# Optimization experiments

Measured on AMD Instinct MI355X. Metric: run time of the kernel, lower is better.

## Reference

```python
import jax, jax.numpy as jnp
import numpy as np

T, B = 32, 64
D_IN = 512      # input_size == embedding dim
H = 512         # hidden_size
V = 32000       # n_vocab
F_FEAT = 768    # feature_size
NH = 8          # num_heads
HD = H // NH    # head_dim


def setup_inputs() -> dict:
    key = jax.random.key(0)
    ks = jax.random.split(key, 16)
    s = 0.02
    inp = {
        'y': jax.random.randint(ks[0], (T, B), 0, V),
        'ctx': jax.random.normal(ks[1], (1, B, F_FEAT), jnp.float32),
        'emb_W': jax.random.normal(ks[2], (V, D_IN), jnp.float32) * s,
        # GRUCell dec0: gates ordered (r, z, n) as in torch
        'W_ih': jax.random.normal(ks[3], (3 * H, D_IN), jnp.float32) * s,
        'b_ih': jnp.zeros((3 * H,), jnp.float32),
        'W_hh': jax.random.normal(ks[4], (3 * H, H), jnp.float32) * s,
        'b_hh': jnp.zeros((3 * H,), jnp.float32),
        # FF att: feature_size -> hidden, tanh
        'W_att': jax.random.normal(ks[5], (H, F_FEAT), jnp.float32) * s,
        'b_att': jnp.zeros((H,), jnp.float32),
        # MultiHeadSelfAttention projections (hidden -> hidden)
        'Wq': jax.random.normal(ks[6], (H, H), jnp.float32) * s,
        'bq': jnp.zeros((H,), jnp.float32),
        'Wk': jax.random.normal(ks[7], (H, H), jnp.float32) * s,
        'bk': jnp.zeros((H,), jnp.float32),
        'Wv': jax.random.normal(ks[8], (H, H), jnp.float32) * s,
        'bv': jnp.zeros((H,), jnp.float32),
        'Wfc': jax.random.normal(ks[9], (H, H), jnp.float32) * s,
        'bfc': jnp.zeros((H,), jnp.float32),
        # FF hid2out: hidden -> input, tanh, bias_zero
        'W_h2o': jax.random.normal(ks[10], (D_IN, H), jnp.float32) * s,
        'b_h2o': jnp.zeros((D_IN,), jnp.float32),
        # FF out2prob: input -> vocab, linear
        'W_out': jax.random.normal(ks[11], (V, D_IN), jnp.float32) * s,
        'b_out': jnp.zeros((V,), jnp.float32),
    }
    return inp


def reference(y, ctx, emb_W, W_ih, b_ih, W_hh, b_hh, W_att, b_att,
              Wq, bq, Wk, bk, Wv, bv, Wfc, bfc, W_h2o, b_h2o, W_out, b_out):
    y_emb = emb_W[y]                                   # [T, B, D_IN]
    # ct is constant across decode steps: tanh FF over pooled image feature
    ct = jnp.tanh(ctx[0] @ W_att.T + b_att)            # [B, H]
    h0 = jnp.zeros((y.shape[1], H), y_emb.dtype)       # dec_init 'zero'

    def step(h, y_t):
        # torch GRUCell (gate order r, z, n)
        gi = y_t @ W_ih.T + b_ih                       # [B, 3H]
        gh = h @ W_hh.T + b_hh                         # [B, 3H]
        gi_r, gi_z, gi_n = jnp.split(gi, 3, axis=-1)
        gh_r, gh_z, gh_n = jnp.split(gh, 3, axis=-1)
        r = jax.nn.sigmoid(gi_r + gh_r)
        z = jax.nn.sigmoid(gi_z + gh_z)
        n = jnp.tanh(gi_n + r * gh_n)
        h1 = (1.0 - z) * n + z * h                     # [B, H]

        x = h1 * ct                                    # [B, H]
        # MultiHeadSelfAttention on a single vector, heads act as sequence
        q = (x @ Wq.T + bq).reshape(-1, NH, HD)        # [B, NH, HD]
        k = (x @ Wk.T + bk).reshape(-1, NH, HD)
        v = (x @ Wv.T + bv).reshape(-1, NH, HD)
        scores = jnp.einsum('bhd,bgd->bhg', q, k) / HD  # note: /head_dim (not sqrt)
        attw = jax.nn.softmax(scores, axis=-1)
        att_out = jnp.einsum('bhg,bgd->bhd', attw, v).reshape(-1, H)
        h2 = att_out @ Wfc.T + bfc                     # [B, H] (fc_out, vocab_size==H)

        logit = jnp.tanh(h2 @ W_h2o.T + b_h2o)         # [B, D_IN]
        prob = jax.nn.softmax(logit @ W_out.T + b_out, axis=-1)  # [B, V]
        return h1, prob                                # f_next returns h1 as next state

    _, probs = jax.lax.scan(step, h0, y_emb)           # [T, B, V]
    return probs
```

## Files before the change

### kernel.cpp

```cpp
#include <hip/hip_runtime.h>
#include <hip/hip_bf16.h>
#include <math.h>

typedef __bf16 bf16_t;
typedef __bf16 bf16x8 __attribute__((ext_vector_type(8)));
typedef __bf16 bf16x4 __attribute__((ext_vector_type(4)));
typedef float  f32x4  __attribute__((ext_vector_type(4)));

#define T_STEPS 32
#define BATCH   64
#define DIN     512
#define HID     512
#define VOCAB   32000
#define FFEAT   768
#define ROWS    2048
#define G3      1536
#define NBLK_A  32

#define EPI_F32  0
#define EPI_BF16 1
#define EPI_TANH 2
#define EPI_SUM  3
#define EPI_PROB 4

#define GLOAD16(gp, lp) __builtin_amdgcn_global_load_lds( \
    (const __attribute__((address_space(1))) void*)(gp),  \
    (__attribute__((address_space(3))) void*)(lp), 16, 0, 0)

#define PHASEV(BUF, MH, NH, STAGE_STMT, GATE_STMT)                            \
  {                                                                           \
    bf16x8 af_[8], bf_[4];                                                    \
    _Pragma("unroll")                                                         \
    for (int m2 = 0; m2 < 4; ++m2) {                                          \
      const int row = wm * 64 + m2 * 16 + la;                                 \
      _Pragma("unroll")                                                       \
      for (int ks = 0; ks < 2; ++ks) {                                        \
        const int sl = (ks * 4 + lg) ^ (row & 7);                             \
        af_[m2 * 2 + ks] =                                                    \
            *(const bf16x8*)&lds[((BUF)*4 + (MH)) * 8192 + row * 64 + sl * 8];\
      }                                                                       \
    }                                                                         \
    _Pragma("unroll")                                                         \
    for (int n2 = 0; n2 < 2; ++n2) {                                          \
      const int row = wn * 32 + n2 * 16 + la;                                 \
      _Pragma("unroll")                                                       \
      for (int ks = 0; ks < 2; ++ks) {                                        \
        const int sl = (ks * 4 + lg) ^ (row & 7);                             \
        bf_[n2 * 2 + ks] =                                                    \
            *(const bf16x8*)&lds[((BUF)*4 + 2 + (NH)) * 8192 + row * 64 + sl * 8];\
      }                                                                       \
    }                                                                         \
    STAGE_STMT;                                                               \
    GATE_STMT;                                                                \
    __builtin_amdgcn_s_barrier();                                             \
    __builtin_amdgcn_s_setprio(1);                                            \
    _Pragma("unroll")                                                         \
    for (int m2 = 0; m2 < 4; ++m2)                                            \
      _Pragma("unroll")                                                       \
      for (int n2 = 0; n2 < 2; ++n2)                                          \
        _Pragma("unroll")                                                     \
        for (int ks = 0; ks < 2; ++ks)                                        \
          acc[(MH)*4 + m2][(NH)*2 + n2] =                                     \
              __builtin_amdgcn_mfma_f32_16x16x32_bf16(                        \
                  af_[m2*2+ks], bf_[n2*2+ks],                                 \
                  acc[(MH)*4 + m2][(NH)*2 + n2], 0, 0, 0);                    \
    __builtin_amdgcn_s_setprio(0);                                            \
    __builtin_amdgcn_s_barrier();                                             \
  }

template<int EPI>
__global__ __launch_bounds__(512, 2) void gemm_v(
    const bf16_t* __restrict__ A, const bf16_t* __restrict__ B,
    const float* __restrict__ bias, float* __restrict__ out,
    float* __restrict__ partial, const float* __restrict__ rowsum,
    int M, int N, int K, int NB)
{
  __shared__ bf16_t lds[2 * 4 * 8192];
  __shared__ float psum[256][4];
  const int tid = threadIdx.x;
  const int lane = tid & 63, wv = tid >> 6;
  const int wm = wv >> 2, wn = wv & 3;
  const int la = lane & 15, lg = lane >> 4;

  const int lin = blockIdx.x;
  const int mt = M >> 8;
  const int cpx = (NB * mt) >> 3;
  const int wg = (lin & 7) * cpx + (lin >> 3);
  const int bn = wg / mt, bm = wg - bn * mt;

  auto stageA = [&](int buf, int h, int kt) {
    const size_t base = (size_t)(bm * 256 + h * 128) * K + (size_t)kt * 64;
#pragma unroll
    for (int q = 0; q < 2; ++q) {
      const int L = q * 512 + tid;
      const int row = L >> 3, sl = L & 7;
      const int c = sl ^ (row & 7);
      GLOAD16(A + base + (size_t)row * K + c * 8,
              &lds[(buf * 4 + h) * 8192 + L * 8]);
    }
  };
  auto stageB = [&](int buf, int h, int kt) {
    const size_t base = (size_t)(bn * 256 + h * 128) * K + (size_t)kt * 64;
#pragma unroll
    for (int q = 0; q < 2; ++q) {
      const int L = q * 512 + tid;
      const int row = L >> 3, sl = L & 7;
      const int c = sl ^ (row & 7);
      GLOAD16(B + base + (size_t)row * K + c * 8,
              &lds[(buf * 4 + 2 + h) * 8192 + L * 8]);
    }
  };

  f32x4 acc[8][4] = {};
  const int NITER = K >> 7;

  stageA(0, 0, 0); stageB(0, 0, 0); stageA(0, 1, 0); stageB(0, 1, 0);
  stageA(1, 0, 1); stageB(1, 0, 1);
  asm volatile("s_waitcnt vmcnt(4)" ::: "memory");
  __builtin_amdgcn_s_barrier();

  for (int it = 0; it < NITER; ++it) {
    const int t0 = 2 * it;
    const bool lastI = (it == NITER - 1);
    PHASEV(0, 0, 0, { stageA(1, 1, t0 + 1); }, ;)
    PHASEV(0, 0, 1, { stageB(1, 1, t0 + 1); }, ;)
    PHASEV(0, 1, 0, { if (!lastI) stageA(0, 0, t0 + 2); }, ;)
    PHASEV(0, 1, 1, { if (!lastI) stageB(0, 0, t0 + 2); },
           { if (lastI) { asm volatile("s_waitcnt vmcnt(0)" ::: "memory"); }
             else       { asm volatile("s_waitcnt vmcnt(4)" ::: "memory"); } })
    PHASEV(1, 0, 0, { if (!lastI) stageA(0, 1, t0 + 2); }, ;)
    PHASEV(1, 0, 1, { if (!lastI) stageB(0, 1, t0 + 2); }, ;)
    PHASEV(1, 1, 0, { if (!lastI) stageA(1, 0, t0 + 3); }, ;)
    PHASEV(1, 1, 1, { if (!lastI) stageB(1, 0, t0 + 3); },
           { if (!lastI) { asm volatile("s_waitcnt vmcnt(4)" ::: "memory"); } })
  }

  float bv[4];
#pragma unroll
  for (int nj = 0; nj < 4; ++nj) {
    const int col = bn * 256 + (nj >> 1) * 128 + wn * 32 + (nj & 1) * 16 + la;
    bv[nj] = bias[col];
  }
#pragma unroll
  for (int mi = 0; mi < 8; ++mi) {
#pragma unroll
    for (int rr = 0; rr < 4; ++rr) {
      const int rowl = (mi >> 2) * 128 + wm * 64 + (mi & 3) * 16 + lg * 4 + rr;
      const int row = bm * 256 + rowl;
      float vsum = 0.f, inv;
      if constexpr (EPI == EPI_PROB) inv = 1.0f / rowsum[row];
#pragma unroll
      for (int nj = 0; nj < 4; ++nj) {
        const float v = acc[mi][nj][rr] + bv[nj];
        if constexpr (EPI == EPI_SUM) {
          vsum += expf(v);
        } else {
          const int col = bn * 256 + (nj >> 1) * 128 + wn * 32 + (nj & 1) * 16 + la;
          out[(size_t)row * N + col] = expf(v) * inv;
        }
      }
      if constexpr (EPI == EPI_SUM) {
        vsum += __shfl_xor(vsum, 1);
        vsum += __shfl_xor(vsum, 2);
        vsum += __shfl_xor(vsum, 4);
        vsum += __shfl_xor(vsum, 8);
        if (la == 0) psum[rowl][wn] = vsum;
      }
    }
  }
  if constexpr (EPI == EPI_SUM) {
    __syncthreads();
    if (tid < 256) {
      partial[(size_t)(bm * 256 + tid) * NB + bn] =
          psum[tid][0] + psum[tid][1] + psum[tid][2] + psum[tid][3];
    }
  }
  (void)out; (void)partial; (void)rowsum;
}

template<int EPI>
__global__ __launch_bounds__(256) void gemm_lds(
    const bf16_t* __restrict__ A, const bf16_t* __restrict__ B,
    const float* __restrict__ bias, void* __restrict__ out,
    int M, int N, int K)
{
  __shared__ bf16_t As[3][128 * 32];
  __shared__ bf16_t Bs[3][128 * 32];

  const int lane = threadIdx.x & 63;
  const int wv   = threadIdx.x >> 6;
  const int wm = wv >> 1, wn = wv & 1;
  const int bn = blockIdx.x, bm = blockIdx.y;
  const int la = lane & 15, lg = lane >> 4;
  const int tid = threadIdx.x;

  auto stage = [&](int buf, int k0) {
#pragma unroll
    for (int q = 0; q < 2; ++q) {
      const int idx = q * 256 + tid;
      const int row = idx >> 2, c = idx & 3;
      const int gch = c ^ ((row >> 1) & 3);
      GLOAD16(A + (size_t)(bm * 128 + row) * K + k0 + gch * 8, &As[buf][idx * 8]);
      GLOAD16(B + (size_t)(bn * 128 + row) * K + k0 + gch * 8, &Bs[buf][idx * 8]);
    }
  };
  const int rdch = (lg ^ ((la >> 1) & 3)) * 8;

  f32x4 acc[4][4] = {};
  const int NT = K >> 5;
  stage(0, 0);
  stage(1, 32);
  for (int kt = 0; kt < NT; ++kt) {
    if (kt + 1 < NT) {
      asm volatile("s_waitcnt vmcnt(4)" ::: "memory");
    } else {
      asm volatile("s_waitcnt vmcnt(0)" ::: "memory");
    }
    __builtin_amdgcn_s_barrier();
    __builtin_amdgcn_sched_barrier(0);
    if (kt + 2 < NT) stage((kt + 2) % 3, (kt + 2) * 32);
    const bf16_t* Ab = As[kt % 3];
    const bf16_t* Bb = Bs[kt % 3];
    bf16x8 a[4], b[4];
#pragma unroll
    for (int i = 0; i < 4; ++i)
      a[i] = *(const bf16x8*)(Ab + (wm * 64 + i * 16 + la) * 32 + rdch);
#pragma unroll
    for (int j = 0; j < 4; ++j)
      b[j] = *(const bf16x8*)(Bb + (wn * 64 + j * 16 + la) * 32 + rdch);
    __builtin_amdgcn_s_setprio(1);
#pragma unroll
    for (int i = 0; i < 4; ++i)
#pragma unroll
      for (int j = 0; j < 4; ++j)
        acc[i][j] = __builtin_amdgcn_mfma_f32_16x16x32_bf16(a[i], b[j], acc[i][j], 0, 0, 0);
    __builtin_amdgcn_s_setprio(0);
  }

  const int m0 = bm * 128 + wm * 64;
  const int n0 = bn * 128 + wn * 64;
  float bv4[4];
#pragma unroll
  for (int j = 0; j < 4; ++j) bv4[j] = bias[n0 + j * 16 + la];
#pragma unroll
  for (int i = 0; i < 4; ++i) {
#pragma unroll
    for (int r = 0; r < 4; ++r) {
      const int row = m0 + i * 16 + lg * 4 + r;
#pragma unroll
      for (int j = 0; j < 4; ++j) {
        const int col = n0 + j * 16 + la;
        float v = acc[i][j][r] + bv4[j];
        if constexpr (EPI == EPI_F32) {
          ((float*)out)[(size_t)row * N + col] = v;
        } else if constexpr (EPI == EPI_BF16) {
          ((bf16_t*)out)[(size_t)row * N + col] = (bf16_t)v;
        } else {
          ((bf16_t*)out)[(size_t)row * N + col] = (bf16_t)tanhf(v);
        }
      }
    }
  }
}

__global__ __launch_bounds__(256) void phaseA_k(
    const bf16_t* __restrict__ Wg, const float* __restrict__ bhh,
    const float* __restrict__ gi, const float* __restrict__ ct,
    unsigned int* __restrict__ hbuf, bf16_t* __restrict__ Xall,
    int* __restrict__ flags, const float* __restrict__ Wout_f32,
    bf16_t* __restrict__ WoutB)
{
  __shared__ bf16_t Wl[48 * 520];
  __shared__ float bl[48];
  const int tid = threadIdx.x, blk = blockIdx.x;

  if (blk >= NBLK_A) {
    const int NCB = gridDim.x - NBLK_A;
    const int n4 = VOCAB * DIN / 4;
    for (int i = (blk - NBLK_A) * 256 + tid; i < n4; i += NCB * 256) {
      float4 v = ((const float4*)Wout_f32)[i];
      bf16x4 o = {(bf16_t)v.x, (bf16_t)v.y, (bf16_t)v.z, (bf16_t)v.w};
      *(bf16x4*)(WoutB + (size_t)i * 4) = o;
    }
    return;
  }

  for (int i = tid; i < 48 * 64; i += 256) {
    const int rw = i >> 6, ch = (i & 63) << 3;
    *(bf16x8*)(Wl + rw * 520 + ch) = *(const bf16x8*)(Wg + (size_t)(blk * 48 + rw) * 512 + ch);
  }
  if (tid < 48) bl[tid] = bhh[blk * 48 + tid];
  __syncthreads();

  const int lane = tid & 63, wv = tid >> 6;
  const int la = lane & 15, lg = lane >> 4;
  const int jcol = blk * 16 + la;
  const int rowA = wv * 16 + la;

  const float blr = bl[la], blz = bl[16 + la], bln = bl[32 + la];
  float hprev[4], ctv[4];
#pragma unroll
  for (int r = 0; r < 4; ++r) {
    hprev[r] = 0.f;
    ctv[r] = ct[(size_t)(wv * 16 + lg * 4 + r) * HID + jcol];
  }

  for (int t = 0; t < T_STEPS; ++t) {
    const float* girow = gi + (size_t)t * BATCH * G3 + (size_t)blk * 48;
    float gv[12];
#pragma unroll
    for (int r = 0; r < 4; ++r) {
      const float* gp = girow + (size_t)(wv * 16 + lg * 4 + r) * G3;
      gv[r * 3 + 0] = gp[la];
      gv[r * 3 + 1] = gp[16 + la];
      gv[r * 3 + 2] = gp[32 + la];
    }
    if (t > 0) {
      if (lane < 32) {
        while (__hip_atomic_load(&flags[(lane * 4 + wv) * 16], __ATOMIC_RELAXED,
                                 __HIP_MEMORY_SCOPE_AGENT) < t)
          __builtin_amdgcn_s_sleep(1);
      }
      asm volatile("" ::: "memory");
    }
    const unsigned long long* hb =
        (const unsigned long long*)(hbuf + (size_t)(t & 1) * 16384);
    bf16x8 af[16];
#pragma unroll
    for (int q = 0; q < 16; ++q) {
      union { unsigned long long u[2]; bf16x8 v; } c;
      const size_t bidx = (size_t)(2 * q + (lg >> 1)) * 256 + rowA * 4 + (lg & 1) * 2;
      c.u[0] = __hip_atomic_load(hb + bidx,     __ATOMIC_RELAXED, __HIP_MEMORY_SCOPE_AGENT);
      c.u[1] = __hip_atomic_load(hb + bidx + 1, __ATOMIC_RELAXED, __HIP_MEMORY_SCOPE_AGENT);
      af[q] = c.v;
    }
    f32x4 acc0 = {}, acc1 = {}, acc2 = {};
#pragma unroll
    for (int q = 0; q < 16; ++q) {
      const bf16_t* wp = Wl + q * 32 + lg * 8;
      bf16x8 b0 = *(const bf16x8*)(wp + (0 * 16 + la) * 520);
      bf16x8 b1 = *(const bf16x8*)(wp + (1 * 16 + la) * 520);
      bf16x8 b2 = *(const bf16x8*)(wp + (2 * 16 + la) * 520);
      acc0 = __builtin_amdgcn_mfma_f32_16x16x32_bf16(af[q], b0, acc0, 0, 0, 0);
      acc1 = __builtin_amdgcn_mfma_f32_16x16x32_bf16(af[q], b1, acc1, 0, 0, 0);
      acc2 = __builtin_amdgcn_mfma_f32_16x16x32_bf16(af[q], b2, acc2, 0, 0, 0);
    }
    float h1v[4];
#pragma unroll
    for (int r = 0; r < 4; ++r) {
      const float ghr = acc0[r] + blr;
      const float ghz = acc1[r] + blz;
      const float ghn = acc2[r] + bln;
      const float rr = 1.f / (1.f + expf(-(gv[r * 3 + 0] + ghr)));
      const float zz = 1.f / (1.f + expf(-(gv[r * 3 + 1] + ghz)));
      const float nn = tanhf(gv[r * 3 + 2] + rr * ghn);
      h1v[r] = (1.f - zz) * nn + zz * hprev[r];
      hprev[r] = h1v[r];
    }
    unsigned int* hn = hbuf + (size_t)((t + 1) & 1) * 16384 + blk * 512;
#pragma unroll
    for (int r = 0; r < 4; ++r) {
      const int row = wv * 16 + lg * 4 + r;
      const unsigned int mine =
          (unsigned int)__builtin_bit_cast(unsigned short, (bf16_t)h1v[r]);
      const unsigned int other = (unsigned int)__shfl_xor((int)mine, 1);
      if ((la & 1) == 0) {
        __hip_atomic_store(hn + row * 8 + (la >> 1), mine | (other << 16),
                           __ATOMIC_RELAXED, __HIP_MEMORY_SCOPE_AGENT);
      }
    }
    asm volatile("s_waitcnt vmcnt(0)" ::: "memory");
    if (lane == 0) {
      __hip_atomic_store(&flags[(blk * 4 + wv) * 16], t + 1, __ATOMIC_RELAXED,
                         __HIP_MEMORY_SCOPE_AGENT);
    }
#pragma unroll
    for (int r = 0; r < 4; ++r) {
      const int row = wv * 16 + lg * 4 + r;
      Xall[((size_t)t * BATCH + row) * HID + jcol] = (bf16_t)(h1v[r] * ctv[r]);
    }
  }
}

__global__ __launch_bounds__(256) void attn_k(const bf16_t* __restrict__ QKV,
                                              bf16_t* __restrict__ attO)
{
  __shared__ float sq[4][512], sk[4][512], sv[4][512], sw[4][64];
  const int tid = threadIdx.x;
  const int wv = tid >> 6, lane = tid & 63;
  const int row = blockIdx.x * 4 + wv;
  const bf16_t* base = QKV + (size_t)row * G3;
  bf16x8 vq = *(const bf16x8*)(base + lane * 8);
  bf16x8 vk = *(const bf16x8*)(base + 512 + lane * 8);
  bf16x8 vv = *(const bf16x8*)(base + 1024 + lane * 8);
#pragma unroll
  for (int e = 0; e < 8; ++e) {
    sq[wv][lane * 8 + e] = (float)vq[e];
    sk[wv][lane * 8 + e] = (float)vk[e];
    sv[wv][lane * 8 + e] = (float)vv[e];
  }
  __syncthreads();
  const int h = lane >> 3, g = lane & 7;
  float s = 0.f;
#pragma unroll 16
  for (int d = 0; d < 64; ++d) s += sq[wv][h * 64 + d] * sk[wv][g * 64 + d];
  s *= (1.f / 64.f);
  float m = s;
  m = fmaxf(m, __shfl_xor(m, 1));
  m = fmaxf(m, __shfl_xor(m, 2));
  m = fmaxf(m, __shfl_xor(m, 4));
  const float e = expf(s - m);
  float sum = e;
  sum += __shfl_xor(sum, 1);
  sum += __shfl_xor(sum, 2);
  sum += __shfl_xor(sum, 4);
  sw[wv][lane] = e / sum;
  __syncthreads();
#pragma unroll
  for (int rep = 0; rep < 8; ++rep) {
    const int idx = rep * 64 + lane;
    const int hh = idx >> 6, d = idx & 63;
    float o = 0.f;
#pragma unroll
    for (int gg = 0; gg < 8; ++gg) o += sw[wv][hh * 8 + gg] * sv[wv][gg * 64 + d];
    attO[(size_t)row * HID + idx] = (bf16_t)o;
  }
}

__global__ __launch_bounds__(256) void cast_k(const float* __restrict__ src,
                                              bf16_t* __restrict__ dst, int n4)
{
  const int i = blockIdx.x * 256 + threadIdx.x;
  if (i >= n4) return;
  float4 v = ((const float4*)src)[i];
  bf16x4 o = {(bf16_t)v.x, (bf16_t)v.y, (bf16_t)v.z, (bf16_t)v.w};
  *(bf16x4*)(dst + (size_t)i * 4) = o;
}

__global__ __launch_bounds__(256) void perm_cast_k(const float* __restrict__ src,
                                                   bf16_t* __restrict__ dst)
{
  const int i = blockIdx.x * 256 + threadIdx.x;
  const int pg = i >> 7, kq = (i & 127) << 2;
  const int g = pg / 48, rem = pg - g * 48, sec = rem >> 4, jj = rem & 15;
  const int srow = sec * 512 + g * 16 + jj;
  float4 v = *(const float4*)(src + (size_t)srow * DIN + kq);
  bf16x4 o = {(bf16_t)v.x, (bf16_t)v.y, (bf16_t)v.z, (bf16_t)v.w};
  *(bf16x4*)(dst + (size_t)pg * DIN + kq) = o;
}

__global__ void perm_bias_k(const float* __restrict__ bih, const float* __restrict__ bhh,
                            float* __restrict__ bihp, float* __restrict__ bhhp)
{
  const int pg = blockIdx.x * 256 + threadIdx.x;
  if (pg >= G3) return;
  const int g = pg / 48, rem = pg - g * 48, sec = rem >> 4, jj = rem & 15;
  const int srow = sec * 512 + g * 16 + jj;
  bihp[pg] = bih[srow];
  bhhp[pg] = bhh[srow];
}

__global__ void bcat_k(const float* __restrict__ a, const float* __restrict__ b,
                       const float* __restrict__ c, float* __restrict__ d)
{
  const int i = blockIdx.x * 256 + threadIdx.x;
  if (i >= G3) return;
  d[i] = i < 512 ? a[i] : (i < 1024 ? b[i - 512] : c[i - 1024]);
}

__global__ __launch_bounds__(256) void yemb_k(const int* __restrict__ y,
                                              const float* __restrict__ embW,
                                              bf16_t* __restrict__ out)
{
  const int idx = blockIdx.x * 256 + threadIdx.x;
  const int rb = idx >> 6, c = (idx & 63) << 3;
  const int tok = y[rb];
  const float4* s = (const float4*)(embW + (size_t)tok * DIN + c);
  float4 v0 = s[0], v1 = s[1];
  bf16x8 o = {(bf16_t)v0.x, (bf16_t)v0.y, (bf16_t)v0.z, (bf16_t)v0.w,
              (bf16_t)v1.x, (bf16_t)v1.y, (bf16_t)v1.z, (bf16_t)v1.w};
  *(bf16x8*)(out + (size_t)rb * DIN + c) = o;
}

__global__ __launch_bounds__(256) void ct_k(const float* __restrict__ ctx,
                                            const float* __restrict__ Watt,
                                            const float* __restrict__ batt,
                                            float* __restrict__ ct)
{
  const int idx = blockIdx.x * 256 + threadIdx.x;
  const int b = idx >> 9, j = idx & 511;
  const float4* c4 = (const float4*)(ctx + (size_t)b * FFEAT);
  const float4* w4 = (const float4*)(Watt + (size_t)j * FFEAT);
  float s = batt[j];
  for (int q = 0; q < FFEAT / 4; ++q) {
    float4 cc = c4[q], ww = w4[q];
    s += cc.x * ww.x + cc.y * ww.y + cc.z * ww.z + cc.w * ww.w;
  }
  ct[idx] = tanhf(s);
}

__global__ __launch_bounds__(256) void reduce_rows(const float* __restrict__ partial,
                                                   float* __restrict__ rowsum, int NB)
{
  const int wv = threadIdx.x >> 6, lane = threadIdx.x & 63;
  const int row = blockIdx.x * 4 + wv;
  float s = 0.f;
  for (int c = lane; c < NB; c += 64) s += partial[(size_t)row * NB + c];
  for (int m = 1; m < 64; m <<= 1) s += __shfl_xor(s, m);
  if (lane == 0) rowsum[row] = s;
}

extern "C" void kernel_launch(void* const* d_in, const int* in_sizes, int n_in,
                              void* d_out, int out_size, void* d_ws, size_t ws_size,
                              hipStream_t stream)
{
  const int*   y     = (const int*)  d_in[0];
  const float* ctx   = (const float*)d_in[1];
  const float* embW  = (const float*)d_in[2];
  const float* W_ih  = (const float*)d_in[3];
  const float* b_ih  = (const float*)d_in[4];
  const float* W_hh  = (const float*)d_in[5];
  const float* b_hh  = (const float*)d_in[6];
  const float* W_att = (const float*)d_in[7];
  const float* b_att = (const float*)d_in[8];
  const float* Wq    = (const float*)d_in[9];
  const float* bq    = (const float*)d_in[10];
  const float* Wk    = (const float*)d_in[11];
  const float* bk    = (const float*)d_in[12];
  const float* Wv    = (const float*)d_in[13];
  const float* bv    = (const float*)d_in[14];
  const float* Wfc   = (const float*)d_in[15];
  const float* bfc   = (const float*)d_in[16];
  const float* Wh2o  = (const float*)d_in[17];
  const float* bh2o  = (const float*)d_in[18];
  const float* W_out = (const float*)d_in[19];
  const float* b_out = (const float*)d_in[20];

  char* p = (char*)d_ws;
  auto alloc = [&](size_t bytes) {
    char* r = p;
    p += (bytes + 255) & ~(size_t)255;
    return r;
  };
  bf16_t* WoutB   = (bf16_t*)alloc((size_t)VOCAB * DIN * 2);
  bf16_t* WgIh    = (bf16_t*)alloc((size_t)G3 * DIN * 2);
  bf16_t* WgHh    = (bf16_t*)alloc((size_t)G3 * DIN * 2);
  bf16_t* Wqkv    = (bf16_t*)alloc((size_t)G3 * DIN * 2);
  bf16_t* WfcB    = (bf16_t*)alloc((size_t)HID * HID * 2);
  bf16_t* Wh2oB   = (bf16_t*)alloc((size_t)HID * HID * 2);
  float*  bIhP    = (float*)alloc(G3 * 4);
  float*  bHhP    = (float*)alloc(G3 * 4);
  float*  bQkv    = (float*)alloc(G3 * 4);
  bf16_t* Yemb    = (bf16_t*)alloc((size_t)ROWS * DIN * 2);
  float*  giP     = (float*)alloc((size_t)ROWS * G3 * 4);
  float*  ctB     = (float*)alloc((size_t)BATCH * HID * 4);
  unsigned int* hbuf = (unsigned int*)alloc((size_t)2 * 16384 * 4);
  bf16_t* Xall    = (bf16_t*)alloc((size_t)ROWS * DIN * 2);
  bf16_t* QKV     = (bf16_t*)alloc((size_t)ROWS * G3 * 2);
  bf16_t* attO    = (bf16_t*)alloc((size_t)ROWS * HID * 2);
  bf16_t* h2B     = (bf16_t*)alloc((size_t)ROWS * HID * 2);
  bf16_t* logit   = (bf16_t*)alloc((size_t)ROWS * DIN * 2);
  float*  partial = (float*)alloc((size_t)ROWS * 250 * 4);
  float*  rowsum  = (float*)alloc((size_t)ROWS * 4);
  int*    flags   = (int*)alloc(32 * 4 * 64);

  hipMemsetAsync(hbuf, 0, (size_t)2 * 16384 * 4, stream);
  hipMemsetAsync(flags, 0, 32 * 4 * 64, stream);

  cast_k<<<256, 256, 0, stream>>>(Wq, Wqkv, HID * HID / 4);
  cast_k<<<256, 256, 0, stream>>>(Wk, Wqkv + (size_t)HID * DIN, HID * HID / 4);
  cast_k<<<256, 256, 0, stream>>>(Wv, Wqkv + (size_t)2 * HID * DIN, HID * HID / 4);
  cast_k<<<256, 256, 0, stream>>>(Wfc, WfcB, HID * HID / 4);
  cast_k<<<256, 256, 0, stream>>>(Wh2o, Wh2oB, HID * HID / 4);
  perm_cast_k<<<768, 256, 0, stream>>>(W_ih, WgIh);
  perm_cast_k<<<768, 256, 0, stream>>>(W_hh, WgHh);
  perm_bias_k<<<6, 256, 0, stream>>>(b_ih, b_hh, bIhP, bHhP);
  bcat_k<<<6, 256, 0, stream>>>(bq, bk, bv, bQkv);
  yemb_k<<<512, 256, 0, stream>>>(y, embW, Yemb);
  ct_k<<<128, 256, 0, stream>>>(ctx, W_att, b_att, ctB);

  gemm_lds<EPI_F32><<<dim3(12, 16), 256, 0, stream>>>(
      Yemb, WgIh, bIhP, giP, ROWS, G3, DIN);

  phaseA_k<<<224, 256, 0, stream>>>(WgHh, bHhP, giP, ctB, hbuf, Xall, flags,
                                    W_out, WoutB);

  gemm_lds<EPI_BF16><<<dim3(12, 16), 256, 0, stream>>>(
      Xall, Wqkv, bQkv, QKV, ROWS, G3, DIN);

  attn_k<<<512, 256, 0, stream>>>(QKV, attO);

  gemm_lds<EPI_BF16><<<dim3(4, 16), 256, 0, stream>>>(
      attO, WfcB, bfc, h2B, ROWS, HID, HID);

  gemm_lds<EPI_TANH><<<dim3(4, 16), 256, 0, stream>>>(
      h2B, Wh2oB, bh2o, logit, ROWS, DIN, HID);

  gemm_v<EPI_SUM><<<1000, 512, 0, stream>>>(
      logit, WoutB, b_out, nullptr, partial, nullptr, ROWS, VOCAB, DIN, 125);
  reduce_rows<<<512, 256, 0, stream>>>(partial, rowsum, 125);
  gemm_v<EPI_PROB><<<1000, 512, 0, stream>>>(
      logit, WoutB, b_out, (float*)d_out, nullptr, rowsum, ROWS, VOCAB, DIN, 125);
}
```

Measured before the change: 492.1 us.

## Cache bf16 exp logits instead of recomputing vocab GEMM; merge cast kernels

Runs the vocab GEMM once and writes exp(logit) to a bf16 cache while accumulating row sums. A separate normalize kernel then rescales the cache into the fp32 output. This replaces the second full GEMM pass and adds a 131 MB write plus read of bf16 data, and it lowers precision of the output to bf16 mantissa. It also folds the five cast launches into one kernel, makes K a template constant with an unrolled loop, and removes the sleep in the spin-wait.

```diff
diff --git a/kernel.cpp b/kernel.cpp
--- a/kernel.cpp
+++ b/kernel.cpp
@@ -20,8 +20,6 @@
 #define EPI_F32  0
 #define EPI_BF16 1
 #define EPI_TANH 2
-#define EPI_SUM  3
-#define EPI_PROB 4
 
 #define GLOAD16(gp, lp) __builtin_amdgcn_global_load_lds( \
     (const __attribute__((address_space(1))) void*)(gp),  \
@@ -68,12 +66,11 @@
     __builtin_amdgcn_s_barrier();                                             \
   }
 
-template<int EPI>
+template<int KD>
 __global__ __launch_bounds__(512, 2) void gemm_v(
     const bf16_t* __restrict__ A, const bf16_t* __restrict__ B,
-    const float* __restrict__ bias, float* __restrict__ out,
-    float* __restrict__ partial, const float* __restrict__ rowsum,
-    int M, int N, int K, int NB)
+    const float* __restrict__ bias, bf16_t* __restrict__ ecache,
+    float* __restrict__ partial, int M, int N, int NB)
 {
   __shared__ bf16_t lds[2 * 4 * 8192];
   __shared__ float psum[256][4];
@@ -89,36 +86,37 @@
   const int bn = wg / mt, bm = wg - bn * mt;
 
   auto stageA = [&](int buf, int h, int kt) {
-    const size_t base = (size_t)(bm * 256 + h * 128) * K + (size_t)kt * 64;
+    const size_t base = (size_t)(bm * 256 + h * 128) * KD + (size_t)kt * 64;
 #pragma unroll
     for (int q = 0; q < 2; ++q) {
       const int L = q * 512 + tid;
       const int row = L >> 3, sl = L & 7;
       const int c = sl ^ (row & 7);
-      GLOAD16(A + base + (size_t)row * K + c * 8,
+      GLOAD16(A + base + (size_t)row * KD + c * 8,
               &lds[(buf * 4 + h) * 8192 + L * 8]);
     }
   };
   auto stageB = [&](int buf, int h, int kt) {
-    const size_t base = (size_t)(bn * 256 + h * 128) * K + (size_t)kt * 64;
+    const size_t base = (size_t)(bn * 256 + h * 128) * KD + (size_t)kt * 64;
 #pragma unroll
     for (int q = 0; q < 2; ++q) {
       const int L = q * 512 + tid;
       const int row = L >> 3, sl = L & 7;
       const int c = sl ^ (row & 7);
-      GLOAD16(B + base + (size_t)row * K + c * 8,
+      GLOAD16(B + base + (size_t)row * KD + c * 8,
               &lds[(buf * 4 + 2 + h) * 8192 + L * 8]);
     }
   };
 
   f32x4 acc[8][4] = {};
-  const int NITER = K >> 7;
+  constexpr int NITER = KD >> 7;
 
   stageA(0, 0, 0); stageB(0, 0, 0); stageA(0, 1, 0); stageB(0, 1, 0);
   stageA(1, 0, 1); stageB(1, 0, 1);
   asm volatile("s_waitcnt vmcnt(4)" ::: "memory");
   __builtin_amdgcn_s_barrier();
 
+#pragma unroll
   for (int it = 0; it < NITER; ++it) {
     const int t0 = 2 * it;
     const bool lastI = (it == NITER - 1);
@@ -147,42 +145,32 @@
     for (int rr = 0; rr < 4; ++rr) {
       const int rowl = (mi >> 2) * 128 + wm * 64 + (mi & 3) * 16 + lg * 4 + rr;
       const int row = bm * 256 + rowl;
-      float vsum = 0.f, inv;
-      if constexpr (EPI == EPI_PROB) inv = 1.0f / rowsum[row];
+      float vsum = 0.f;
 #pragma unroll
       for (int nj = 0; nj < 4; ++nj) {
-        const float v = acc[mi][nj][rr] + bv[nj];
-        if constexpr (EPI == EPI_SUM) {
-          vsum += expf(v);
-        } else {
-          const int col = bn * 256 + (nj >> 1) * 128 + wn * 32 + (nj & 1) * 16 + la;
-          out[(size_t)row * N + col] = expf(v) * inv;
-        }
+        const float e = expf(acc[mi][nj][rr] + bv[nj]);
+        const int col = bn * 256 + (nj >> 1) * 128 + wn * 32 + (nj & 1) * 16 + la;
+        ecache[(size_t)row * N + col] = (bf16_t)e;
+        vsum += e;
       }
-      if constexpr (EPI == EPI_SUM) {
-        vsum += __shfl_xor(vsum, 1);
-        vsum += __shfl_xor(vsum, 2);
-        vsum += __shfl_xor(vsum, 4);
-        vsum += __shfl_xor(vsum, 8);
-        if (la == 0) psum[rowl][wn] = vsum;
-      }
-    }
-  }
-  if constexpr (EPI == EPI_SUM) {
-    __syncthreads();
-    if (tid < 256) {
-      partial[(size_t)(bm * 256 + tid) * NB + bn] =
-          psum[tid][0] + psum[tid][1] + psum[tid][2] + psum[tid][3];
-    }
-  }
-  (void)out; (void)partial; (void)rowsum;
-}
-
-template<int EPI>
+      vsum += __shfl_xor(vsum, 1);
+      vsum += __shfl_xor(vsum, 2);
+      vsum += __shfl_xor(vsum, 4);
+      vsum += __shfl_xor(vsum, 8);
+      if (la == 0) psum[rowl][wn] = vsum;
+    }
+  }
+  __syncthreads();
+  if (tid < 256) {
+    partial[(size_t)(bm * 256 + tid) * NB + bn] =
+        psum[tid][0] + psum[tid][1] + psum[tid][2] + psum[tid][3];
+  }
+}
+
+template<int EPI, int KD>
 __global__ __launch_bounds__(256) void gemm_lds(
     const bf16_t* __restrict__ A, const bf16_t* __restrict__ B,
-    const float* __restrict__ bias, void* __restrict__ out,
-    int M, int N, int K)
+    const float* __restrict__ bias, void* __restrict__ out, int M, int N)
 {
   __shared__ bf16_t As[3][128 * 32];
   __shared__ bf16_t Bs[3][128 * 32];
@@ -200,14 +188,14 @@
       const int idx = q * 256 + tid;
       const int row = idx >> 2, c = idx & 3;
       const int gch = c ^ ((row >> 1) & 3);
-      GLOAD16(A + (size_t)(bm * 128 + row) * K + k0 + gch * 8, &As[buf][idx * 8]);
-      GLOAD16(B + (size_t)(bn * 128 + row) * K + k0 + gch * 8, &Bs[buf][idx * 8]);
+      GLOAD16(A + (size_t)(bm * 128 + row) * KD + k0 + gch * 8, &As[buf][idx * 8]);
+      GLOAD16(B + (size_t)(bn * 128 + row) * KD + k0 + gch * 8, &Bs[buf][idx * 8]);
     }
   };
   const int rdch = (lg ^ ((la >> 1) & 3)) * 8;
 
   f32x4 acc[4][4] = {};
-  const int NT = K >> 5;
+  constexpr int NT = KD >> 5;
   stage(0, 0);
   stage(1, 32);
   for (int kt = 0; kt < NT; ++kt) {
@@ -318,8 +306,7 @@
     if (t > 0) {
       if (lane < 32) {
         while (__hip_atomic_load(&flags[(lane * 4 + wv) * 16], __ATOMIC_RELAXED,
-                                 __HIP_MEMORY_SCOPE_AGENT) < t)
-          __builtin_amdgcn_s_sleep(1);
+                                 __HIP_MEMORY_SCOPE_AGENT) < t) { }
       }
       asm volatile("" ::: "memory");
     }
@@ -427,11 +414,18 @@
   }
 }
 
-__global__ __launch_bounds__(256) void cast_k(const float* __restrict__ src,
-                                              bf16_t* __restrict__ dst, int n4)
-{
-  const int i = blockIdx.x * 256 + threadIdx.x;
-  if (i >= n4) return;
+__global__ __launch_bounds__(256) void cast5_k(
+    const float* __restrict__ s0, const float* __restrict__ s1,
+    const float* __restrict__ s2, const float* __restrict__ s3,
+    const float* __restrict__ s4, bf16_t* __restrict__ Wqkv,
+    bf16_t* __restrict__ WfcB, bf16_t* __restrict__ Wh2oB)
+{
+  const int seg = blockIdx.x >> 8;
+  const int i = (blockIdx.x & 255) * 256 + threadIdx.x;
+  const float* src = seg == 0 ? s0 : seg == 1 ? s1 : seg == 2 ? s2
+                   : seg == 3 ? s3 : s4;
+  bf16_t* dst = seg <= 2 ? Wqkv + (size_t)seg * HID * DIN
+              : seg == 3 ? WfcB : Wh2oB;
   float4 v = ((const float4*)src)[i];
   bf16x4 o = {(bf16_t)v.x, (bf16_t)v.y, (bf16_t)v.z, (bf16_t)v.w};
   *(bf16x4*)(dst + (size_t)i * 4) = o;
@@ -508,6 +502,22 @@
   for (int c = lane; c < NB; c += 64) s += partial[(size_t)row * NB + c];
   for (int m = 1; m < 64; m <<= 1) s += __shfl_xor(s, m);
   if (lane == 0) rowsum[row] = s;
+}
+
+__global__ __launch_bounds__(256) void normalize_k(const bf16_t* __restrict__ e,
+                                                   const float* __restrict__ rowsum,
+                                                   float* __restrict__ out)
+{
+  const int row = blockIdx.y;
+  const int c8 = blockIdx.x * 256 + threadIdx.x;
+  if (c8 >= VOCAB / 8) return;
+  const float inv = 1.0f / rowsum[row];
+  const size_t base = (size_t)row * VOCAB + (size_t)c8 * 8;
+  bf16x8 v = *(const bf16x8*)(e + base);
+  float4 o0 = {(float)v[0] * inv, (float)v[1] * inv, (float)v[2] * inv, (float)v[3] * inv};
+  float4 o1 = {(float)v[4] * inv, (float)v[5] * inv, (float)v[6] * inv, (float)v[7] * inv};
+  *(float4*)(out + base) = o0;
+  *(float4*)(out + base + 4) = o1;
 }
 
 extern "C" void kernel_launch(void* const* d_in, const int* in_sizes, int n_in,
@@ -560,18 +570,15 @@
   bf16_t* attO    = (bf16_t*)alloc((size_t)ROWS * HID * 2);
   bf16_t* h2B     = (bf16_t*)alloc((size_t)ROWS * HID * 2);
   bf16_t* logit   = (bf16_t*)alloc((size_t)ROWS * DIN * 2);
-  float*  partial = (float*)alloc((size_t)ROWS * 250 * 4);
+  float*  partial = (float*)alloc((size_t)ROWS * 125 * 4);
   float*  rowsum  = (float*)alloc((size_t)ROWS * 4);
   int*    flags   = (int*)alloc(32 * 4 * 64);
+  bf16_t* eCache  = (bf16_t*)alloc((size_t)ROWS * VOCAB * 2);
 
   hipMemsetAsync(hbuf, 0, (size_t)2 * 16384 * 4, stream);
   hipMemsetAsync(flags, 0, 32 * 4 * 64, stream);
 
-  cast_k<<<256, 256, 0, stream>>>(Wq, Wqkv, HID * HID / 4);
-  cast_k<<<256, 256, 0, stream>>>(Wk, Wqkv + (size_t)HID * DIN, HID * HID / 4);
-  cast_k<<<256, 256, 0, stream>>>(Wv, Wqkv + (size_t)2 * HID * DIN, HID * HID / 4);
-  cast_k<<<256, 256, 0, stream>>>(Wfc, WfcB, HID * HID / 4);
-  cast_k<<<256, 256, 0, stream>>>(Wh2o, Wh2oB, HID * HID / 4);
+  cast5_k<<<1280, 256, 0, stream>>>(Wq, Wk, Wv, Wfc, Wh2o, Wqkv, WfcB, Wh2oB);
   perm_cast_k<<<768, 256, 0, stream>>>(W_ih, WgIh);
   perm_cast_k<<<768, 256, 0, stream>>>(W_hh, WgHh);
   perm_bias_k<<<6, 256, 0, stream>>>(b_ih, b_hh, bIhP, bHhP);
@@ -579,26 +586,25 @@
   yemb_k<<<512, 256, 0, stream>>>(y, embW, Yemb);
   ct_k<<<128, 256, 0, stream>>>(ctx, W_att, b_att, ctB);
 
-  gemm_lds<EPI_F32><<<dim3(12, 16), 256, 0, stream>>>(
-      Yemb, WgIh, bIhP, giP, ROWS, G3, DIN);
+  gemm_lds<EPI_F32, DIN><<<dim3(12, 16), 256, 0, stream>>>(
+      Yemb, WgIh, bIhP, giP, ROWS, G3);
 
   phaseA_k<<<224, 256, 0, stream>>>(WgHh, bHhP, giP, ctB, hbuf, Xall, flags,
                                     W_out, WoutB);
 
-  gemm_lds<EPI_BF16><<<dim3(12, 16), 256, 0, stream>>>(
-      Xall, Wqkv, bQkv, QKV, ROWS, G3, DIN);
+  gemm_lds<EPI_BF16, DIN><<<dim3(12, 16), 256, 0, stream>>>(
+      Xall, Wqkv, bQkv, QKV, ROWS, G3);
 
   attn_k<<<512, 256, 0, stream>>>(QKV, attO);
 
-  gemm_lds<EPI_BF16><<<dim3(4, 16), 256, 0, stream>>>(
-      attO, WfcB, bfc, h2B, ROWS, HID, HID);
-
-  gemm_lds<EPI_TANH><<<dim3(4, 16), 256, 0, stream>>>(
-      h2B, Wh2oB, bh2o, logit, ROWS, DIN, HID);
-
-  gemm_v<EPI_SUM><<<1000, 512, 0, stream>>>(
-      logit, WoutB, b_out, nullptr, partial, nullptr, ROWS, VOCAB, DIN, 125);
+  gemm_lds<EPI_BF16, HID><<<dim3(4, 16), 256, 0, stream>>>(
+      attO, WfcB, bfc, h2B, ROWS, HID);
+
+  gemm_lds<EPI_TANH, HID><<<dim3(4, 16), 256, 0, stream>>>(
+      h2B, Wh2oB, bh2o, logit, ROWS, DIN);
+
+  gemm_v<DIN><<<1000, 512, 0, stream>>>(
+      logit, WoutB, b_out, eCache, partial, ROWS, VOCAB, 125);
   reduce_rows<<<512, 256, 0, stream>>>(partial, rowsum, 125);
-  gemm_v<EPI_PROB><<<1000, 512, 0, stream>>>(
-      logit, WoutB, b_out, (float*)d_out, nullptr, rowsum, ROWS, VOCAB, DIN, 125);
-}
+  normalize_k<<<dim3(16, ROWS), 256, 0, stream>>>(eCache, rowsum, (float*)d_out);
+}
```

After: 442.2 us. 10.1% less time.
